# Optimization experiments

Measured on AMD Instinct MI355X. Metric: run time of the kernel, lower is better.

The kernel has to match this reference:

```python
import jax, jax.numpy as jnp
import numpy as np

# Shapes hard-coded by the original module
B, C1, C2, S, K, H, E = 128, 128, 14, 14, 3, 256, 2  # batch, chan-split, chan-split, spatial, kernel, hidden, expand


def setup_inputs() -> dict:
    key = jax.random.key(0)
    k1, k2, k3 = jax.random.split(key, 3)
    x = jax.random.normal(k1, (B, C1 * C2, S), dtype=jnp.float32)
    w0 = jax.random.normal(k2, (H, E), dtype=jnp.float32)        # weights[0]
    w1 = jax.random.normal(k3, (C1, K, H), dtype=jnp.float32)    # weights[1]
    return {"x": x, "w0": w0, "w1": w1, "shift": 1}


def reference(x, w0, w1, shift):
    # reshape to (B, C1, C2, S); original torch treats it as (B, 1792, 14, 1)
    xr = x.reshape(B, C1, C2, S)
    # unfold((3,1), padding=(1,0)): 1D im2col along the S (=14) axis
    xp = jnp.pad(xr, ((0, 0), (0, 0), (0, 0), (1, 1)))
    # patches[b, j, n, i, m] = xp[b, j, n, m + i]  -> (B, C1, C2, K, S)
    patches = jnp.stack([xp[..., k:k + S] for k in range(K)], axis=3)
    # einsum 'ljnmi,jik->lnmk' (torch had m,i swapped via permute; fold it in)
    t4 = jnp.einsum('ljnim,jik->lnmk', patches, w1)   # (B, C2, S, H)
    # einsum 'kmlj,ji->kmlji': outer product with w0 along a new expand dim
    t5 = t4[..., None] * w0                            # (B, C2, S, H, E)
    t5 = jnp.roll(t5, shift, axis=1)                   # cyclic shift over C2
    t6 = jnp.transpose(t5, (0, 2, 3, 1, 4)).reshape(B, S, H, C2 * E)
    t6 = jnp.roll(t6, shift, axis=3)                   # cyclic shift over merged (C2*E)
    t6 = t6.reshape(B, S, H, C2, E).sum(axis=4)        # (B, S, H, C2)
    return jnp.transpose(t6, (0, 2, 3, 1))             # (B, H, C2, S) = (128, 256, 14, 14)
```

## Files before the change

kernel.cpp:

```cpp
#include <hip/hip_runtime.h>
#include <hip/hip_bf16.h>
#include <math.h>

#define B_   128
#define C1_  128
#define C2_  14
#define S_   14
#define K_   3
#define H_   256
#define E_   2

#define HT   64
#define NT   4
#define XROWS 224
#define XSTR 72
#define BSTR 200
#define CROW 228

typedef unsigned short u16;
typedef unsigned int   u32;
typedef __attribute__((ext_vector_type(8))) short bf16x8;
typedef __attribute__((ext_vector_type(4))) float f32x4;

__device__ __forceinline__ u16 f2bf(float f) {
    u32 u = __float_as_uint(f);
    return (u16)((u + 0x7FFF + ((u >> 16) & 1)) >> 16);
}

__device__ __forceinline__ int decode_shift(const int* p) {
    int a = p[0];
    if (a >= -100 && a <= 100 && a != 0) return a;
    float f = __int_as_float(a);
    if (f >= -100.f && f <= 100.f && f == truncf(f) && f != 0.f) return (int)f;
    long long bits = ((long long)p[1] << 32) | (unsigned int)a;
    double d = __longlong_as_double(bits);
    if (d >= -100.0 && d <= 100.0 && d == trunc(d) && d != 0.0) return (int)d;
    return a;
}

__global__ __launch_bounds__(256) void cvt_kernel(const float* __restrict__ x,
                                                  const float* __restrict__ w1,
                                                  u16* __restrict__ xg,
                                                  u16* __restrict__ wg) {
    const int blk = blockIdx.x;
    const int t   = threadIdx.x;
    if (blk < 1024) {
        __shared__ u16 xl[64 * 50];
        const int b   = blk >> 3;
        const int hf  = (blk >> 2) & 1;
        const int qr  = blk & 3;
        const int cs0 = qr * 49;
        const float* xb = x + (size_t)(b * C1_ + hf * 64) * 196 + cs0;
#pragma unroll
        for (int i = 0; i < 13; ++i) {
            int idx = t + 256 * i;
            if (idx < 3136) {
                int c1l = idx / 49, j = idx - c1l * 49;
                xl[c1l * 50 + j] = f2bf(xb[c1l * 196 + j]);
            }
        }
        __syncthreads();
        u16* dst = xg + ((size_t)(b * 2 + hf) * XROWS + qr * 56) * 64;
#pragma unroll
        for (int i = 0; i < 2; ++i) {
            int task = t + 256 * i;
            if (task < 448) {
                int rr = task >> 3, o = task & 7;
                int row = qr * 56 + rr;
                int p = row & 15;
                uint4 val = make_uint4(0, 0, 0, 0);
                if (p >= 1 && p <= 14) {
                    int csl = (row >> 4) * 14 + p - 1 - cs0;
                    u16 v[8];
#pragma unroll
                    for (int j = 0; j < 8; ++j) v[j] = xl[(o * 8 + j) * 50 + csl];
                    val.x = (u32)v[0] | ((u32)v[1] << 16);
                    val.y = (u32)v[2] | ((u32)v[3] << 16);
                    val.z = (u32)v[4] | ((u32)v[5] << 16);
                    val.w = (u32)v[6] | ((u32)v[7] << 16);
                }
                *(uint4*)&dst[(size_t)rr * 64 + o * 8] = val;
            }
        }
    } else {
        int q = (blk - 1024) * 256 + t;
        float4 v = ((const float4*)w1)[q];
        int i0 = q * 4;
        int c1 = i0 / 768;
        int kk = (i0 - c1 * 768) >> 8;
        int h0 = i0 & 255;
        int hf = c1 >> 6, c1l = c1 & 63;
        u16 b4[4] = { f2bf(v.x), f2bf(v.y), f2bf(v.z), f2bf(v.w) };
#pragma unroll
        for (int d = 0; d < 4; ++d) {
            int h = h0 + d, g = h >> 6, hl = h & 63;
            wg[(size_t)((g * 2 + hf) * 64 + hl) * 192 + kk * 64 + c1l] = b4[d];
        }
    }
}

__global__ __launch_bounds__(256, 2) void fused_kernel(const u16* __restrict__ xg,
                                                       const float* __restrict__ w0,
                                                       const u16* __restrict__ wg,
                                                       const int* __restrict__ shift_p,
                                                       float* __restrict__ out) {
    __shared__ __align__(16) char lds[58368];
    u16*   xT = (u16*)lds;
    u16*   Bt = (u16*)(lds + 32544);
    float* Cl = (float*)lds;

    const int b    = blockIdx.x >> 2;
    const int g    = blockIdx.x & 3;
    const int h0   = g * HT;
    const int t    = threadIdx.x;
    const int wave = t >> 6;
    const int lane = t & 63;
    const int quad = lane >> 4;
    const int l15  = lane & 15;

    f32x4 acc[4][NT];
#pragma unroll
    for (int i = 0; i < 4; ++i)
#pragma unroll
        for (int j = 0; j < NT; ++j) acc[i][j] = (f32x4){0.f, 0.f, 0.f, 0.f};

    for (int hf = 0; hf < 2; ++hf) {
        if (hf) __syncthreads();
        {
            const uint4* src = (const uint4*)(xg + (size_t)(b * 2 + hf) * (XROWS * 64));
#pragma unroll
            for (int i = 0; i < 7; ++i) {
                int idx = t + 256 * i;
                uint4 v = src[idx];
                *(uint4*)&xT[(idx >> 3) * XSTR + (idx & 7) * 8] = v;
            }
        }
        {
            const uint4* src = (const uint4*)(wg + (size_t)(g * 2 + hf) * (64 * 192));
#pragma unroll
            for (int i = 0; i < 6; ++i) {
                int idx = t + 256 * i;
                uint4 v = src[idx];
                int hl = idx / 24, co = idx - hl * 24;
                *(uint4*)&Bt[hl * BSTR + co * 8] = v;
            }
        }
        __syncthreads();

#pragma unroll
        for (int tt = 0; tt < 6; ++tt) {
            const int kk = tt >> 1;
            const int coff = (tt & 1) * 32 + quad * 8;
            bf16x8 bfr[NT];
#pragma unroll
            for (int nc = 0; nc < NT; ++nc)
                bfr[nc] = *(const bf16x8*)&Bt[(nc * 16 + l15) * BSTR + kk * 64 + coff];
#pragma unroll
            for (int mi = 0; mi < 4; ++mi) {
                int mt = wave + mi * 4;
                if (mt < 14) {
                    int r = mt * 16 + l15;
                    bf16x8 af = *(const bf16x8*)&xT[(r + kk) * XSTR + coff];
#pragma unroll
                    for (int nc = 0; nc < NT; ++nc)
                        acc[mi][nc] = __builtin_amdgcn_mfma_f32_16x16x32_bf16(
                            af, bfr[nc], acc[mi][nc], 0, 0, 0);
                }
            }
        }
    }

    __syncthreads();
#pragma unroll
    for (int mi = 0; mi < 4; ++mi) {
        int mt = wave + mi * 4;
        if (mt < 14) {
#pragma unroll
            for (int nc = 0; nc < NT; ++nc) {
                int hl = nc * 16 + l15;
                *(f32x4*)&Cl[hl * CROW + mt * 16 + quad * 4] = acc[mi][nc];
            }
        }
    }
    __syncthreads();

    const int shift = decode_shift(shift_p);
    const int hl = t >> 2, sub = t & 3;
    const int h = h0 + hl;
    int c0[2]; float wv[2];
#pragma unroll
    for (int e = 0; e < 2; ++e) {
        int q = (e - shift) % 28; if (q < 0) q += 28;
        int np0 = q >> 1, ep = q & 1;
        int c = (np0 - shift) % 14; if (c < 0) c += 14;
        c0[e] = c;
        wv[e] = w0[h * 2 + ep];
    }
    const float* Crow = &Cl[hl * CROW];
    float* orow = out + (size_t)(b * H_ + h) * 196;
#pragma unroll
    for (int jj = 0; jj < 13; ++jj) {
        int i = sub + 4 * jj;
        if (i < 49) {
            float tmp[4];
#pragma unroll
            for (int e4 = 0; e4 < 4; ++e4) {
                int idx = 4 * i + e4;
                int n = idx / 14, m = idx - n * 14;
                int cA = c0[0] + n; if (cA >= 14) cA -= 14;
                int cB = c0[1] + n; if (cB >= 14) cB -= 14;
                tmp[e4] = wv[0] * Crow[cA * 16 + m] + wv[1] * Crow[cB * 16 + m];
            }
            *(float4*)&orow[4 * i] = make_float4(tmp[0], tmp[1], tmp[2], tmp[3]);
        }
    }
}

__global__ __launch_bounds__(256) void t4_fb(const float* __restrict__ x,
                                             const float* __restrict__ w1,
                                             float* __restrict__ t4) {
    __shared__ float xl[C1_][16];
    const int b = blockIdx.x / C2_, c2 = blockIdx.x % C2_, h = threadIdx.x;
    for (int i = h; i < C1_ * S_; i += 256) {
        int c1 = i / S_, s = i % S_;
        xl[c1][s + 1] = x[((size_t)(b * C1_ + c1) * C2_ + c2) * S_ + s];
    }
    if (h < C1_) { xl[h][0] = 0.f; xl[h][15] = 0.f; }
    __syncthreads();
    float acc[S_];
#pragma unroll
    for (int s = 0; s < S_; ++s) acc[s] = 0.f;
    for (int c1 = 0; c1 < C1_; ++c1) {
        float wa = w1[(size_t)(c1 * K_ + 0) * H_ + h];
        float wb = w1[(size_t)(c1 * K_ + 1) * H_ + h];
        float wc = w1[(size_t)(c1 * K_ + 2) * H_ + h];
#pragma unroll
        for (int s = 0; s < S_; ++s)
            acc[s] += wa * xl[c1][s] + wb * xl[c1][s + 1] + wc * xl[c1][s + 2];
    }
    size_t base = ((size_t)(b * H_ + h) * C2_ + c2) * S_;
#pragma unroll
    for (int s = 0; s < S_; ++s) t4[base + s] = acc[s];
}
__global__ __launch_bounds__(224) void out_fb(float* __restrict__ t4,
                                              const float* __restrict__ w0,
                                              const int* __restrict__ shift_p) {
    const int tid = threadIdx.x;
    const int m = tid % S_, hh = tid / S_;
    const int b = blockIdx.x / 16, h = (blockIdx.x % 16) * 16 + hh;
    const int shift = decode_shift(shift_p);
    const size_t colbase = ((size_t)(b * H_ + h) * C2_) * S_ + m;
    float tl[C2_];
#pragma unroll
    for (int c2 = 0; c2 < C2_; ++c2) tl[c2] = t4[colbase + (size_t)c2 * S_];
    const float w0v[2] = { w0[h * 2 + 0], w0[h * 2 + 1] };
    float r[C2_];
#pragma unroll
    for (int n = 0; n < C2_; ++n) {
        float a = 0.f;
#pragma unroll
        for (int e = 0; e < 2; ++e) {
            int q = (2 * n + e - shift) % 28; if (q < 0) q += 28;
            int np = q >> 1, ep = q & 1;
            int c2 = (np - shift) % 14; if (c2 < 0) c2 += 14;
            a += tl[c2] * w0v[ep];
        }
        r[n] = a;
    }
#pragma unroll
    for (int n = 0; n < C2_; ++n) t4[colbase + (size_t)n * S_] = r[n];
}

extern "C" void kernel_launch(void* const* d_in, const int* in_sizes, int n_in,
                              void* d_out, int out_size, void* d_ws, size_t ws_size,
                              hipStream_t stream) {
    const float* x     = (const float*)d_in[0];
    const float* w0    = (const float*)d_in[1];
    const float* w1    = (const float*)d_in[2];
    const int*   shift = (const int*)(n_in > 3 ? d_in[3] : d_in[n_in - 1]);
    for (int i = 0; i < n_in; ++i) {
        int sz = in_sizes[i];
        if (sz == B_ * C1_ * C2_ * S_)      x     = (const float*)d_in[i];
        else if (sz == H_ * E_)             w0    = (const float*)d_in[i];
        else if (sz == C1_ * K_ * H_)       w1    = (const float*)d_in[i];
        else if (sz == 1)                   shift = (const int*)d_in[i];
    }
    float* out = (float*)d_out;

    const size_t NXG = (size_t)B_ * 2 * XROWS * 64;
    const size_t NWG = (size_t)4 * 2 * 64 * 192;
    if (ws_size >= (NXG + NWG) * sizeof(u16)) {
        u16* xg = (u16*)d_ws;
        u16* wg = xg + NXG;
        cvt_kernel<<<1024 + 96, 256, 0, stream>>>(x, w1, xg, wg);
        fused_kernel<<<B_ * 4, 256, 0, stream>>>(xg, w0, wg, shift, out);
    } else {
        t4_fb<<<B_ * C2_, 256, 0, stream>>>(x, w1, out);
        out_fb<<<B_ * 16, 224, 0, stream>>>(out, w0, shift);
    }
}
```

Measured before the change: 89.91 us.

## Load GEMM tiles via async global-to-LDS with XOR-swizzled layouts and XCD-aware block mapping

Replaces the register-staged global->LDS copies of the x and weight tiles with global_load_lds async 16-byte transfers. Because those transfers cannot apply padded strides, the producer kernel now writes both tensors in an XOR-swizzled chunk order, and the MFMA operand reads apply the matching XOR to avoid LDS bank conflicts. Block indices are also remapped so that the blocks for a given batch land on the same XCD, for better L2 locality. This relies on correct wait semantics for async LDS loads before __syncthreads and adds coupling between the layouts of the two kernels.

```diff
diff --git a/kernel.cpp b/kernel.cpp
--- a/kernel.cpp
+++ b/kernel.cpp
@@ -13,14 +13,17 @@
 #define HT   64
 #define NT   4
 #define XROWS 224
-#define XSTR 72
-#define BSTR 200
+#define BT_OFF 28928
 #define CROW 228
 
 typedef unsigned short u16;
 typedef unsigned int   u32;
 typedef __attribute__((ext_vector_type(8))) short bf16x8;
 typedef __attribute__((ext_vector_type(4))) float f32x4;
+
+#define ASYNC16(g, l) __builtin_amdgcn_global_load_lds(                        \
+    (const __attribute__((address_space(1))) void*)(g),                        \
+    (__attribute__((address_space(3))) void*)(l), 16, 0, 0)
 
 __device__ __forceinline__ u16 f2bf(float f) {
     u32 u = __float_as_uint(f);
@@ -60,7 +63,7 @@
             }
         }
         __syncthreads();
-        u16* dst = xg + ((size_t)(b * 2 + hf) * XROWS + qr * 56) * 64;
+        u16* dst = xg + (size_t)(b * 2 + hf) * (XROWS * 64) + (size_t)qr * 56 * 64;
 #pragma unroll
         for (int i = 0; i < 2; ++i) {
             int task = t + 256 * i;
@@ -79,7 +82,8 @@
                     val.z = (u32)v[4] | ((u32)v[5] << 16);
                     val.w = (u32)v[6] | ((u32)v[7] << 16);
                 }
-                *(uint4*)&dst[(size_t)rr * 64 + o * 8] = val;
+                int op = o ^ (row & 7);
+                *(uint4*)&dst[rr * 64 + op * 8] = val;
             }
         }
     } else {
@@ -90,11 +94,13 @@
         int kk = (i0 - c1 * 768) >> 8;
         int h0 = i0 & 255;
         int hf = c1 >> 6, c1l = c1 & 63;
+        int cb0 = c1l >> 3, j = c1l & 7;
         u16 b4[4] = { f2bf(v.x), f2bf(v.y), f2bf(v.z), f2bf(v.w) };
 #pragma unroll
         for (int d = 0; d < 4; ++d) {
             int h = h0 + d, g = h >> 6, hl = h & 63;
-            wg[(size_t)((g * 2 + hf) * 64 + hl) * 192 + kk * 64 + c1l] = b4[d];
+            int cb = cb0 ^ (hl & 7);
+            wg[(size_t)((g * 2 + hf) * 64 + hl) * 192 + kk * 64 + cb * 8 + j] = b4[d];
         }
     }
 }
@@ -105,18 +111,20 @@
                                                        const int* __restrict__ shift_p,
                                                        float* __restrict__ out) {
     __shared__ __align__(16) char lds[58368];
-    u16*   xT = (u16*)lds;
-    u16*   Bt = (u16*)(lds + 32544);
     float* Cl = (float*)lds;
 
-    const int b    = blockIdx.x >> 2;
-    const int g    = blockIdx.x & 3;
+    const int raw  = blockIdx.x;
+    const int xcd  = raw & 7;
+    const int slot = raw >> 3;
+    const int b    = xcd * 16 + (slot & 15);
+    const int g    = slot >> 4;
     const int h0   = g * HT;
     const int t    = threadIdx.x;
     const int wave = t >> 6;
     const int lane = t & 63;
     const int quad = lane >> 4;
     const int l15  = lane & 15;
+    const int wbase = t & ~63;
 
     f32x4 acc[4][NT];
 #pragma unroll
@@ -126,41 +134,33 @@
 
     for (int hf = 0; hf < 2; ++hf) {
         if (hf) __syncthreads();
-        {
-            const uint4* src = (const uint4*)(xg + (size_t)(b * 2 + hf) * (XROWS * 64));
-#pragma unroll
-            for (int i = 0; i < 7; ++i) {
-                int idx = t + 256 * i;
-                uint4 v = src[idx];
-                *(uint4*)&xT[(idx >> 3) * XSTR + (idx & 7) * 8] = v;
-            }
-        }
-        {
-            const uint4* src = (const uint4*)(wg + (size_t)(g * 2 + hf) * (64 * 192));
-#pragma unroll
-            for (int i = 0; i < 6; ++i) {
-                int idx = t + 256 * i;
-                uint4 v = src[idx];
-                int hl = idx / 24, co = idx - hl * 24;
-                *(uint4*)&Bt[hl * BSTR + co * 8] = v;
-            }
-        }
+        const uint4* xs = (const uint4*)(xg + (size_t)(b * 2 + hf) * (XROWS * 64));
+        const uint4* bs = (const uint4*)(wg + (size_t)(g * 2 + hf) * (64 * 192));
+#pragma unroll
+        for (int i = 0; i < 7; ++i)
+            ASYNC16(xs + 256 * i + t, lds + (size_t)(256 * i + wbase) * 16);
+#pragma unroll
+        for (int i = 0; i < 6; ++i)
+            ASYNC16(bs + 256 * i + t, lds + BT_OFF + (size_t)(256 * i + wbase) * 16);
         __syncthreads();
 
 #pragma unroll
         for (int tt = 0; tt < 6; ++tt) {
-            const int kk = tt >> 1;
-            const int coff = (tt & 1) * 32 + quad * 8;
+            const int kk  = tt >> 1;
+            const int cbl = (tt & 1) * 4 + quad;
+            const int bsw = (cbl ^ (l15 & 7)) << 4;
+            const int asw = (cbl ^ ((l15 + kk) & 7)) << 4;
             bf16x8 bfr[NT];
 #pragma unroll
             for (int nc = 0; nc < NT; ++nc)
-                bfr[nc] = *(const bf16x8*)&Bt[(nc * 16 + l15) * BSTR + kk * 64 + coff];
+                bfr[nc] = *(const bf16x8*)(lds + BT_OFF +
+                            (nc * 16 + l15) * 384 + kk * 128 + bsw);
 #pragma unroll
             for (int mi = 0; mi < 4; ++mi) {
                 int mt = wave + mi * 4;
                 if (mt < 14) {
-                    int r = mt * 16 + l15;
-                    bf16x8 af = *(const bf16x8*)&xT[(r + kk) * XSTR + coff];
+                    int row = mt * 16 + l15 + kk;
+                    bf16x8 af = *(const bf16x8*)(lds + row * 128 + asw);
 #pragma unroll
                     for (int nc = 0; nc < NT; ++nc)
                         acc[mi][nc] = __builtin_amdgcn_mfma_f32_16x16x32_bf16(
```

After: 90.57 us. About the same (+0.7%).
